# Kernel optimization log

Measured on AMD Instinct MI355X. Metric: run time of the kernel, lower is better.

The kernel has to match this reference:

```python
import jax, jax.numpy as jnp
import numpy as np

B, T = 16, 8192
L, RC, DC, SC, EC, E, NC = 16, 32, 32, 256, 256, 100, 256


def conv1d(x, w, b, dilation=1):
    # x: [B, Cin, T], w: [Cout, Cin, K], b: [Cout]
    y = jax.lax.conv_general_dilated(
        x, w, window_strides=(1,), padding='VALID',
        rhs_dilation=(dilation,), dimension_numbers=('NCH', 'OIH', 'NCH'))
    return y + b[None, :, None]


def setup_inputs() -> dict:
    key = jax.random.key(0)
    ks = jax.random.split(key, 32)
    n = lambda k, shp: (jax.random.normal(k, shp) * 0.1).astype(jnp.float32)
    return dict(
        tokens=jax.random.randint(ks[0], (B, T), 0, NC),
        emb=n(ks[1], (NC, E)),
        init_w=n(ks[2], (RC, E, 1)), init_b=n(ks[3], (RC,)),
        dil_w=n(ks[4], (L, DC, RC, 2)), dil_b=n(ks[5], (L, DC)),
        filt_w=n(ks[6], (L, DC, DC, 2)), filt_b=n(ks[7], (L, DC)),
        gate_w=n(ks[8], (L, DC, DC, 2)), gate_b=n(ks[9], (L, DC)),
        res_w=n(ks[10], (L, RC, DC, 1)), res_b=n(ks[11], (L, RC)),
        skip_w=n(ks[12], (L, SC, DC, 1)), skip_b=n(ks[13], (L, SC)),
        end1_w=n(ks[14], (EC, SC, 1)), end1_b=n(ks[15], (EC,)),
        end2_w=n(ks[16], (EC, EC, 1)), end2_b=n(ks[17], (EC,)),
        fc1_w=n(ks[18], (128, 256)), fc1_b=n(ks[19], (128,)),
        fc2_w=n(ks[20], (128, 128)), fc2_b=n(ks[21], (128,)),
        fc3_w=n(ks[22], (64, 128)), fc3_b=n(ks[23], (64,)),
        fc4_w=n(ks[24], (NC, 64)), fc4_b=n(ks[25], (NC,)),
    )


def reference(tokens, emb, init_w, init_b, dil_w, dil_b, filt_w, filt_b,
              gate_w, gate_b, res_w, res_b, skip_w, skip_b,
              end1_w, end1_b, end2_w, end2_b,
              fc1_w, fc1_b, fc2_w, fc2_b, fc3_w, fc3_b, fc4_w, fc4_b):
    x = emb[tokens]                     # [B, T, E]
    x = jnp.transpose(x, (0, 2, 1))     # [B, E, T]
    x = conv1d(x, init_w, init_b)       # [B, RC, T]
    skip = None
    for i in range(L):
        d = 2 ** (i % 4)                # dilation resets each block of 4 layers
        xp = jnp.pad(x, ((0, 0), (0, 0), (d + 1, 0)))        # left pad d+1
        residual = conv1d(xp, dil_w[i], dil_b[i], dilation=d)  # [B, DC, T+1]
        f = jnp.tanh(conv1d(residual, filt_w[i], filt_b[i]))   # [B, DC, T]
        g = jax.nn.sigmoid(conv1d(residual, gate_w[i], gate_b[i]))
        x = f * g
        skip = conv1d(x, skip_w[i], skip_b[i])   # overwritten each layer (source bug, kept faithful)
        x = conv1d(x, res_w[i], res_b[i]) + residual[:, :, :-1]
    h = jax.nn.relu(conv1d(jax.nn.relu(skip), end1_w, end1_b))
    h = conv1d(h, end2_w, end2_b)       # [B, EC, T]
    h = h[:, :, -1]                     # [B, 256] last timestep only
    h = jax.nn.relu(h @ fc1_w.T + fc1_b)
    h = jax.nn.relu(h @ fc2_w.T + fc2_b)
    h = jax.nn.relu(h @ fc3_w.T + fc3_b)
    out = h @ fc4_w.T + fc4_b           # [B, NC]
    return out
```

## Files before the change

kernel.cpp:

```cpp
#include <hip/hip_runtime.h>


#define BB 16
#define TT 8192
#define LL 16
#define W0 77
#define NT 256

typedef __attribute__((ext_vector_type(8)))  short short8;
typedef __attribute__((ext_vector_type(16))) float float16;

#define MFMA_B16(a, b, c) __builtin_amdgcn_mfma_f32_32x32x16_bf16(a, b, c, 0, 0, 0)

__device__ __forceinline__ short f2bs(float f) {
  union { float ff; unsigned u; } v; v.ff = f;
  unsigned u = v.u;
  return (short)((u + 0x7FFFu + ((u >> 16) & 1u)) >> 16);
}
__device__ __forceinline__ float b2f(short h) {
  union { unsigned u; float f; } v;
  v.u = ((unsigned)(unsigned short)h) << 16; return v.f;
}
__device__ __forceinline__ unsigned cvtpk(float lo, float hi) {
  unsigned r;
  asm("v_cvt_pk_bf16_f32 %0, %1, %2" : "=v"(r) : "v"(lo), "v"(hi));
  return r;
}
__device__ __forceinline__ short8 mk8(unsigned a, unsigned b, unsigned c, unsigned d) {
  union { unsigned u[4]; short8 s; } z;
  z.u[0] = a; z.u[1] = b; z.u[2] = c; z.u[3] = d; return z.s;
}
__device__ __forceinline__ float u2f(unsigned u) {
  union { unsigned x; float f; } z; z.x = u; return z.f;
}
__device__ __forceinline__ void asmb(const unsigned* own, const unsigned* cr,
                                     int kh, unsigned* o) {
  #pragma unroll
  for (int h = 0; h < 2; h++) {
    o[4*h+0] = kh ? cr[4*h+2] : own[4*h+0];
    o[4*h+1] = kh ? cr[4*h+3] : own[4*h+1];
    o[4*h+2] = kh ? own[4*h+2] : cr[4*h+0];
    o[4*h+3] = kh ? own[4*h+3] : cr[4*h+1];
  }
}

__device__ __forceinline__ void afrag2(const short* src, int row, int kh, short8* out) {
  out[0] = *(const short8*)&src[row * 32 + 8 * kh];
  out[1] = *(const short8*)&src[row * 32 + 16 + 8 * kh];
}

__device__ __forceinline__ void load_chunk(
    int li, int cid, float* pf,
    const float* dil_w, const float* filt_w, const float* gate_w, const float* res_w)
{
  int mat = cid >> 7;
  int h = (cid >> 6) & 1, ln = cid & 63;
  int n = ln & 31, k2 = ln >> 5;
  int base = (li * 32 + n) * 32 + 16 * h + 8 * k2;
  if (mat == 6) {
    const float* p = res_w + base;
    #pragma unroll
    for (int j = 0; j < 8; j++) pf[j] = p[j];
  } else {
    const float* w = (mat < 2) ? dil_w : (mat < 4) ? filt_w : gate_w;
    const float* p = w + base * 2 + (mat & 1);
    #pragma unroll
    for (int j = 0; j < 8; j++) pf[j] = p[2 * j];
  }
}

__global__ __launch_bounds__(NT, 1) void wavenet_kernel(
    const int* __restrict__ tokens,
    const float* __restrict__ emb,
    const float* __restrict__ init_w, const float* __restrict__ init_b,
    const float* __restrict__ dil_w,  const float* __restrict__ dil_b,
    const float* __restrict__ filt_w, const float* __restrict__ filt_b,
    const float* __restrict__ gate_w, const float* __restrict__ gate_b,
    const float* __restrict__ res_w,  const float* __restrict__ res_b,
    const float* __restrict__ skip_w, const float* __restrict__ skip_b,
    const float* __restrict__ end1_w, const float* __restrict__ end1_b,
    const float* __restrict__ end2_w, const float* __restrict__ end2_b,
    const float* __restrict__ fc1_w,  const float* __restrict__ fc1_b,
    const float* __restrict__ fc2_w,  const float* __restrict__ fc2_b,
    const float* __restrict__ fc3_w,  const float* __restrict__ fc3_b,
    const float* __restrict__ fc4_w,  const float* __restrict__ fc4_b,
    float* __restrict__ out)
{
  __shared__ __align__(16) short bfw[2][7168];
  __shared__ __align__(16) float bias2[2][128];
  __shared__ __align__(16) short xbuf[W0 * 32];
  __shared__ __align__(16) short pool[8624];
  __shared__ int tok[W0];
  __shared__ __align__(16) float vecA[256], vecB[256];

  short* rb = pool;
  short* xm = pool + 2432;

  const int tid  = threadIdx.x;
  const int lane = tid & 63;
  const int wv   = tid >> 6;
  const int m    = lane & 31;
  const int kh   = lane >> 5;
  const int b    = blockIdx.x;

  if (tid < W0) tok[tid] = tokens[b * TT + (TT - 1 - tid)];
  __syncthreads();

  for (int cid = tid; cid < 77 * 14; cid += NT) {
    int u = cid / 14, s = cid % 14;
    const float* er = emb + tok[u] * 100 + s * 8;
    short8 v;
    if (s < 12) {
      #pragma unroll
      for (int j = 0; j < 8; j++) v[j] = f2bs(er[j]);
    } else if (s == 12) {
      #pragma unroll
      for (int j = 0; j < 4; j++) v[j] = f2bs(er[j]);
      #pragma unroll
      for (int j = 4; j < 8; j++) v[j] = 0;
    } else {
      #pragma unroll
      for (int j = 0; j < 8; j++) v[j] = 0;
    }
    *(short8*)&pool[u * 112 + s * 8] = v;
  }
  for (int cid = tid; cid < 896; cid += NT) {
    float pf[8];
    load_chunk(0, cid, pf, dil_w, filt_w, gate_w, res_w);
    short8 v;
    #pragma unroll
    for (int j = 0; j < 8; j++) v[j] = f2bs(pf[j]);
    *(short8*)&bfw[0][cid * 8] = v;
  }
  if (tid < 128) {
    const float* bsrc = (tid < 32) ? dil_b : (tid < 64) ? filt_b : (tid < 96) ? gate_b : res_b;
    bias2[0][tid] = bsrc[tid & 31];
  }
  __syncthreads();

  if (wv < 3) {
    short8 bi[7];
    #pragma unroll
    for (int s = 0; s < 7; s++) {
      const float* p = init_w + m * 100 + s * 16 + kh * 8;
      short8 v;
      if (s < 6) {
        #pragma unroll
        for (int j = 0; j < 8; j++) v[j] = f2bs(p[j]);
      } else if (kh == 0) {
        #pragma unroll
        for (int j = 0; j < 4; j++) v[j] = f2bs(p[j]);
        #pragma unroll
        for (int j = 4; j < 8; j++) v[j] = 0;
      } else {
        #pragma unroll
        for (int j = 0; j < 8; j++) v[j] = 0;
      }
      bi[s] = v;
    }
    const float binit = init_b[m];
    const int R = wv * 32;
    int u = R + m; if (u > 76) u = 76;
    float16 acc;
    #pragma unroll
    for (int r = 0; r < 16; r++) acc[r] = binit;
    #pragma unroll
    for (int s = 0; s < 7; s++) {
      short8 a = *(const short8*)&pool[u * 112 + s * 16 + kh * 8];
      acc = MFMA_B16(a, bi[s], acc);
    }
    #pragma unroll
    for (int r = 0; r < 16; r++) {
      int row = (r & 3) + 8 * (r >> 2) + 4 * kh;
      int uu = R + row;
      if (uu < W0) xbuf[uu * 32 + m] = f2bs(acc[r]);
    }
  }
  __syncthreads();

  int Win = W0;
  for (int i = 0; i < 11; i++) {
    const int d = 1 << (i & 3);
    const int Wout = Win - d - 1;
    const int T = (Wout + 32) >> 5;
    const short* bw = bfw[i & 1];
    const float* bs = bias2[i & 1];

    float pfo[4][8];
    float pbias = 0.f;
    const int nch = (tid < 128) ? 4 : 3;
    const bool oldpf = (T >= 3) && (i + 1 < LL);
    if (oldpf) {
      #pragma unroll
      for (int q = 0; q < 4; q++) {
        if (q < nch)
          load_chunk(i + 1, tid + q * NT, pfo[q], dil_w, filt_w, gate_w, res_w);
      }
      if (tid < 128) {
        const float* bsrc = (tid < 32) ? dil_b : (tid < 64) ? filt_b : (tid < 96) ? gate_b : res_b;
        pbias = bsrc[(i + 1) * 32 + (tid & 31)];
      }
    }
    const bool newpf = (T <= 2) && (i + 1 < LL) && (wv >= T);
    const int nP = NT - T * 64;
    const int ptid = tid - T * 64;
    float pfn[7][8];
    if (newpf) {
      #pragma unroll
      for (int q = 0; q < 7; q++) {
        int c = ptid + q * nP;
        if (c < 896) load_chunk(i + 1, c, pfn[q], dil_w, filt_w, gate_w, res_w);
      }
    }

    short8 BW[5][2];
    if (wv < T) {
      const int R = wv * 32;
      short8 B0[2], B1[2];
      #pragma unroll
      for (int h = 0; h < 2; h++) {
        B0[h] = *(const short8*)&bw[((0 * 2 + h) * 64 + lane) * 8];
        B1[h] = *(const short8*)&bw[((1 * 2 + h) * 64 + lane) * 8];
      }
      #pragma unroll
      for (int mt = 0; mt < 5; mt++)
        #pragma unroll
        for (int h = 0; h < 2; h++)
          BW[mt][h] = *(const short8*)&bw[(((mt + 2) * 2 + h) * 64 + lane) * 8];
      int vra = R + m + d; if (vra > Win - 1) vra = Win - 1;
      int vrz = R + m;     if (vrz > Win - 1) vrz = Win - 1;
      short8 aA[2], aZ[2];
      afrag2(xbuf, vra, kh, aA);
      afrag2(xbuf, vrz, kh, aZ);
      float16 acc;
      const float bc = bs[m];
      #pragma unroll
      for (int r = 0; r < 16; r++) acc[r] = bc;
      acc = MFMA_B16(aA[0], B0[0], acc);
      acc = MFMA_B16(aA[1], B0[1], acc);
      acc = MFMA_B16(aZ[0], B1[0], acc);
      acc = MFMA_B16(aZ[1], B1[1], acc);
      #pragma unroll
      for (int r = 0; r < 16; r++) {
        int row = (r & 3) + 8 * (r >> 2) + 4 * kh;
        int vr = R + row;
        if (vr <= Wout) rb[vr * 32 + m] = f2bs(acc[r]);
      }
    }
    if (T >= 2) {
      __syncthreads();
    } else {
      asm volatile("s_waitcnt lgkmcnt(0)" ::: "memory");
    }

    if (wv < T) {
      const int R = wv * 32;
      int r1 = R + m + 1; if (r1 > Wout) r1 = Wout;
      int r0 = R + m;     if (r0 > Wout) r0 = Wout;
      short8 a1[2], a0[2];
      afrag2(rb, r1, kh, a1);
      afrag2(rb, r0, kh, a0);
      float16 accF, accG;
      const float bf = bs[32 + m], bg = bs[64 + m];
      #pragma unroll
      for (int r = 0; r < 16; r++) { accF[r] = bf; accG[r] = bg; }
      accF = MFMA_B16(a1[0], BW[0][0], accF);
      accF = MFMA_B16(a1[1], BW[0][1], accF);
      accF = MFMA_B16(a0[0], BW[1][0], accF);
      accF = MFMA_B16(a0[1], BW[1][1], accF);
      accG = MFMA_B16(a1[0], BW[2][0], accG);
      accG = MFMA_B16(a1[1], BW[2][1], accG);
      accG = MFMA_B16(a0[0], BW[3][0], accG);
      accG = MFMA_B16(a0[1], BW[3][1], accG);
      #pragma unroll
      for (int r = 0; r < 16; r++) {
        int row = (r & 3) + 8 * (r >> 2) + 4 * kh;
        int uf = R + row;
        if (uf < Wout) {
          float u = __expf(-2.f * accF[r]);
          float v = __expf(-accG[r]);
          float fg = (1.f - u) * __builtin_amdgcn_rcpf((1.f + u) * (1.f + v));
          xm[uf * 32 + m] = f2bs(fg);
        }
      }
      asm volatile("s_waitcnt lgkmcnt(0)" ::: "memory");

      int rx = R + m; if (rx > Wout - 1) rx = Wout - 1;
      short8 aX[2];
      afrag2(xm, rx, kh, aX);
      float16 accX;
      const float br = bs[96 + m];
      #pragma unroll
      for (int r = 0; r < 16; r++) {
        int row = (r & 3) + 8 * (r >> 2) + 4 * kh;
        int rr = R + row + 1; if (rr > Wout) rr = Wout;
        accX[r] = br + b2f(rb[rr * 32 + m]);
      }
      accX = MFMA_B16(aX[0], BW[4][0], accX);
      accX = MFMA_B16(aX[1], BW[4][1], accX);
      #pragma unroll
      for (int r = 0; r < 16; r++) {
        int row = (r & 3) + 8 * (r >> 2) + 4 * kh;
        int uf = R + row;
        if (uf < Wout) xbuf[uf * 32 + m] = f2bs(accX[r]);
      }
    } else if (newpf) {
      short* dst = bfw[(i + 1) & 1];
      #pragma unroll
      for (int q = 0; q < 7; q++) {
        int c = ptid + q * nP;
        if (c < 896) {
          short8 v;
          #pragma unroll
          for (int j = 0; j < 8; j++) v[j] = f2bs(pfn[q][j]);
          *(short8*)&dst[c * 8] = v;
        }
      }
      for (int t2 = ptid; t2 < 128; t2 += nP) {
        const float* bsrc = (t2 < 32) ? dil_b : (t2 < 64) ? filt_b : (t2 < 96) ? gate_b : res_b;
        bias2[(i + 1) & 1][t2] = bsrc[(i + 1) * 32 + (t2 & 31)];
      }
    }

    if (oldpf) {
      short* dst = bfw[(i + 1) & 1];
      #pragma unroll
      for (int q = 0; q < 4; q++) {
        if (q < nch) {
          short8 v;
          #pragma unroll
          for (int j = 0; j < 8; j++) v[j] = f2bs(pfo[q][j]);
          *(short8*)&dst[(tid + q * NT) * 8] = v;
        }
      }
      if (tid < 128) bias2[(i + 1) & 1][tid] = pbias;
    }
    __syncthreads();
    Win = Wout;
  }

  {
    const int t31 = lane & 31;
    const int hb  = lane & 32;
    unsigned xcur[8];
    if (wv == 0) {
      int tcl = t31 < Win - 1 ? t31 : Win - 1;
      #pragma unroll
      for (int h = 0; h < 2; h++) {
        short8 v = *(const short8*)&xbuf[tcl * 32 + 16 * h + 8 * kh];
        union { short8 s; unsigned u[4]; } z; z.s = v;
        #pragma unroll
        for (int s = 0; s < 4; s++) xcur[4 * h + s] = z.u[s];
      }
    }

    #pragma unroll
    for (int i = 11; i < LL; i++) {
      const int d = 1 << (i & 3);
      const int Wout = Win - d - 1;
      const short* bw = bfw[i & 1];
      const float* bs = bias2[i & 1];

      const bool npf = (i + 1 < LL) && (wv >= 1);
      const int ptid = tid - 64;
      float pfn[7][8];
      if (npf) {
        #pragma unroll
        for (int q = 0; q < 7; q++) {
          int c = ptid + q * 192;
          if (c < 896) load_chunk(i + 1, c, pfn[q], dil_w, filt_w, gate_w, res_w);
        }
      }

      if (wv == 0) {
        short8 WA[7][2];
        #pragma unroll
        for (int mt = 0; mt < 7; mt++)
          #pragma unroll
          for (int h = 0; h < 2; h++)
            WA[mt][h] = *(const short8*)&bw[((mt * 2 + h) * 64 + lane) * 8];

        int td = t31 + d; if (td > Win - 1) td = Win - 1;
        int srcd = hb | td;
        unsigned xd[8];
        #pragma unroll
        for (int q = 0; q < 8; q++) xd[q] = (unsigned)__shfl((int)xcur[q], srcd);
        float16 acc;
        #pragma unroll
        for (int g = 0; g < 4; g++) {
          float4 b4 = *(const float4*)&bs[4 * kh + 8 * g];
          acc[4*g+0] = b4.x; acc[4*g+1] = b4.y; acc[4*g+2] = b4.z; acc[4*g+3] = b4.w;
        }
        acc = MFMA_B16(WA[0][0], mk8(xd[0], xd[1], xd[2], xd[3]), acc);
        acc = MFMA_B16(WA[0][1], mk8(xd[4], xd[5], xd[6], xd[7]), acc);
        acc = MFMA_B16(WA[1][0], mk8(xcur[0], xcur[1], xcur[2], xcur[3]), acc);
        acc = MFMA_B16(WA[1][1], mk8(xcur[4], xcur[5], xcur[6], xcur[7]), acc);

        unsigned wrb[8], xc[8], x1[8], x1c[8];
        #pragma unroll
        for (int q = 0; q < 8; q++) wrb[q] = cvtpk(acc[2 * q], acc[2 * q + 1]);
        int t1 = t31 + 1; if (t1 > Wout) t1 = Wout;
        int s1o = hb | t1;
        int s1c = (hb ^ 32) | t1;
        #pragma unroll
        for (int q = 0; q < 8; q++) {
          xc[q]  = (unsigned)__shfl((int)wrb[q], lane ^ 32);
          x1[q]  = (unsigned)__shfl((int)wrb[q], s1o);
          x1c[q] = (unsigned)__shfl((int)wrb[q], s1c);
        }
        unsigned rb0w[8], rb1w[8];
        asmb(wrb, xc, kh, rb0w);
        asmb(x1, x1c, kh, rb1w);

        float16 accF, accG;
        #pragma unroll
        for (int g = 0; g < 4; g++) {
          float4 bF = *(const float4*)&bs[32 + 4 * kh + 8 * g];
          float4 bG = *(const float4*)&bs[64 + 4 * kh + 8 * g];
          accF[4*g+0] = bF.x; accF[4*g+1] = bF.y; accF[4*g+2] = bF.z; accF[4*g+3] = bF.w;
          accG[4*g+0] = bG.x; accG[4*g+1] = bG.y; accG[4*g+2] = bG.z; accG[4*g+3] = bG.w;
        }
        short8 RB10 = mk8(rb1w[0], rb1w[1], rb1w[2], rb1w[3]);
        short8 RB11 = mk8(rb1w[4], rb1w[5], rb1w[6], rb1w[7]);
        short8 RB00 = mk8(rb0w[0], rb0w[1], rb0w[2], rb0w[3]);
        short8 RB01 = mk8(rb0w[4], rb0w[5], rb0w[6], rb0w[7]);
        accF = MFMA_B16(WA[2][0], RB10, accF);
        accF = MFMA_B16(WA[2][1], RB11, accF);
        accF = MFMA_B16(WA[3][0], RB00, accF);
        accF = MFMA_B16(WA[3][1], RB01, accF);
        accG = MFMA_B16(WA[4][0], RB10, accG);
        accG = MFMA_B16(WA[4][1], RB11, accG);
        accG = MFMA_B16(WA[5][0], RB00, accG);
        accG = MFMA_B16(WA[5][1], RB01, accG);
        float fg[16];
        #pragma unroll
        for (int r = 0; r < 16; r++) {
          float u = __expf(-2.f * accF[r]);
          float v = __expf(-accG[r]);
          fg[r] = (1.f - u) * __builtin_amdgcn_rcpf((1.f + u) * (1.f + v));
        }
        unsigned wxm[8];
        #pragma unroll
        for (int q = 0; q < 8; q++) wxm[q] = cvtpk(fg[2 * q], fg[2 * q + 1]);

        if (i == LL - 1) {
          if (t31 == 0) {
            #pragma unroll
            for (int q = 0; q < 8; q++) {
              int c0 = (2 * q & 3) + 8 * (q >> 1) + 4 * kh;
              *(unsigned*)&xm[c0] = wxm[q];
            }
          }
        } else {
          unsigned xmc[8];
          #pragma unroll
          for (int q = 0; q < 8; q++) xmc[q] = (unsigned)__shfl((int)wxm[q], lane ^ 32);
          unsigned xmw[8];
          asmb(wxm, xmc, kh, xmw);
          float16 accX;
          #pragma unroll
          for (int g = 0; g < 4; g++) {
            float4 bR = *(const float4*)&bs[96 + 4 * kh + 8 * g];
            #pragma unroll
            for (int j = 0; j < 4; j++) {
              int r = 4 * g + j;
              unsigned w = x1[r >> 1];
              float rv = (r & 1) ? u2f(w & 0xFFFF0000u) : u2f(w << 16);
              accX[r] = ((const float*)&bR)[j] + rv;
            }
          }
          accX = MFMA_B16(WA[6][0], mk8(xmw[0], xmw[1], xmw[2], xmw[3]), accX);
          accX = MFMA_B16(WA[6][1], mk8(xmw[4], xmw[5], xmw[6], xmw[7]), accX);
          unsigned wxn[8], xnc[8];
          #pragma unroll
          for (int q = 0; q < 8; q++) wxn[q] = cvtpk(accX[2 * q], accX[2 * q + 1]);
          #pragma unroll
          for (int q = 0; q < 8; q++) xnc[q] = (unsigned)__shfl((int)wxn[q], lane ^ 32);
          asmb(wxn, xnc, kh, xcur);
        }
      } else if (npf) {
        short* dst = bfw[(i + 1) & 1];
        #pragma unroll
        for (int q = 0; q < 7; q++) {
          int c = ptid + q * 192;
          if (c < 896) {
            short8 v;
            #pragma unroll
            for (int j = 0; j < 8; j++) v[j] = f2bs(pfn[q][j]);
            *(short8*)&dst[c * 8] = v;
          }
        }
        for (int t2 = ptid; t2 < 128; t2 += 192) {
          const float* bsrc = (t2 < 32) ? dil_b : (t2 < 64) ? filt_b : (t2 < 96) ? gate_b : res_b;
          bias2[(i + 1) & 1][t2] = bsrc[(i + 1) * 32 + (t2 & 31)];
        }
      }
      __syncthreads();
      Win = Wout;
    }
  }

  {
    float acc = skip_b[15 * 256 + tid];
    const float* wr = skip_w + (15 * 256 + tid) * 32;
    #pragma unroll
    for (int k = 0; k < 32; k += 4) {
      float4 w = *(const float4*)&wr[k];
      acc += (w.x * b2f(xm[k]) + w.y * b2f(xm[k+1])) + (w.z * b2f(xm[k+2]) + w.w * b2f(xm[k+3]));
    }
    vecA[tid] = fmaxf(acc, 0.f);
  }
  __syncthreads();
  {
    const float* wr = end1_w + tid * 256;
    float a4[4] = {0.f, 0.f, 0.f, 0.f};
    #pragma unroll 4
    for (int k = 0; k < 256; k += 16) {
      #pragma unroll
      for (int q = 0; q < 4; q++) {
        float4 w = *(const float4*)&wr[k + 4 * q];
        float4 a = *(const float4*)&vecA[k + 4 * q];
        a4[q] += (w.x * a.x + w.y * a.y) + (w.z * a.z + w.w * a.w);
      }
    }
    vecB[tid] = fmaxf(end1_b[tid] + (a4[0] + a4[1]) + (a4[2] + a4[3]), 0.f);
  }
  __syncthreads();
  float h2;
  {
    const float* wr = end2_w + tid * 256;
    float a4[4] = {0.f, 0.f, 0.f, 0.f};
    #pragma unroll 4
    for (int k = 0; k < 256; k += 16) {
      #pragma unroll
      for (int q = 0; q < 4; q++) {
        float4 w = *(const float4*)&wr[k + 4 * q];
        float4 a = *(const float4*)&vecB[k + 4 * q];
        a4[q] += (w.x * a.x + w.y * a.y) + (w.z * a.z + w.w * a.w);
      }
    }
    h2 = end2_b[tid] + (a4[0] + a4[1]) + (a4[2] + a4[3]);
  }
  __syncthreads();
  vecA[tid] = h2;
  __syncthreads();
  if (tid < 128) {
    const float* wr = fc1_w + tid * 256;
    float a4[4] = {0.f, 0.f, 0.f, 0.f};
    #pragma unroll 4
    for (int k = 0; k < 256; k += 16) {
      #pragma unroll
      for (int q = 0; q < 4; q++) {
        float4 w = *(const float4*)&wr[k + 4 * q];
        float4 a = *(const float4*)&vecA[k + 4 * q];
        a4[q] += (w.x * a.x + w.y * a.y) + (w.z * a.z + w.w * a.w);
      }
    }
    vecB[tid] = fmaxf(fc1_b[tid] + (a4[0] + a4[1]) + (a4[2] + a4[3]), 0.f);
  }
  __syncthreads();
  if (tid < 128) {
    const float* wr = fc2_w + tid * 128;
    float a4[4] = {0.f, 0.f, 0.f, 0.f};
    #pragma unroll 2
    for (int k = 0; k < 128; k += 16) {
      #pragma unroll
      for (int q = 0; q < 4; q++) {
        float4 w = *(const float4*)&wr[k + 4 * q];
        float4 a = *(const float4*)&vecB[k + 4 * q];
        a4[q] += (w.x * a.x + w.y * a.y) + (w.z * a.z + w.w * a.w);
      }
    }
    vecA[tid] = fmaxf(fc2_b[tid] + (a4[0] + a4[1]) + (a4[2] + a4[3]), 0.f);
  }
  __syncthreads();
  if (tid < 64) {
    const float* wr = fc3_w + tid * 128;
    float a4[4] = {0.f, 0.f, 0.f, 0.f};
    #pragma unroll 2
    for (int k = 0; k < 128; k += 16) {
      #pragma unroll
      for (int q = 0; q < 4; q++) {
        float4 w = *(const float4*)&wr[k + 4 * q];
        float4 a = *(const float4*)&vecA[k + 4 * q];
        a4[q] += (w.x * a.x + w.y * a.y) + (w.z * a.z + w.w * a.w);
      }
    }
    vecB[tid] = fmaxf(fc3_b[tid] + (a4[0] + a4[1]) + (a4[2] + a4[3]), 0.f);
  }
  __syncthreads();
  {
    const float* wr = fc4_w + tid * 64;
    float a4[4] = {0.f, 0.f, 0.f, 0.f};
    #pragma unroll
    for (int k = 0; k < 64; k += 16) {
      #pragma unroll
      for (int q = 0; q < 4; q++) {
        float4 w = *(const float4*)&wr[k + 4 * q];
        float4 a = *(const float4*)&vecB[k + 4 * q];
        a4[q] += (w.x * a.x + w.y * a.y) + (w.z * a.z + w.w * a.w);
      }
    }
    out[b * 256 + tid] = fc4_b[tid] + (a4[0] + a4[1]) + (a4[2] + a4[3]);
  }
}

extern "C" void kernel_launch(void* const* d_in, const int* in_sizes, int n_in,
                              void* d_out, int out_size, void* d_ws, size_t ws_size,
                              hipStream_t stream) {
  wavenet_kernel<<<BB, NT, 0, stream>>>(
      (const int*)d_in[0],    (const float*)d_in[1],  (const float*)d_in[2],  (const float*)d_in[3],
      (const float*)d_in[4],  (const float*)d_in[5],  (const float*)d_in[6],  (const float*)d_in[7],
      (const float*)d_in[8],  (const float*)d_in[9],  (const float*)d_in[10], (const float*)d_in[11],
      (const float*)d_in[12], (const float*)d_in[13], (const float*)d_in[14], (const float*)d_in[15],
      (const float*)d_in[16], (const float*)d_in[17], (const float*)d_in[18], (const float*)d_in[19],
      (const float*)d_in[20], (const float*)d_in[21], (const float*)d_in[22], (const float*)d_in[23],
      (const float*)d_in[24], (const float*)d_in[25], (float*)d_out);
}
```

Baseline: 205.0 us.

## Overlap 31-row wave tiles to drop intra-layer barrier, double-buffer xbuf

Each wave now owns a 31-row output tile that overlaps its neighbour by one row, so the dilated conv result a wave writes is the only data it later reads. This replaces the block-wide __syncthreads between the dilated and filter/gate stages with a local lgkmcnt wait. The residual output goes into a second, double-buffered xbuf so layers no longer read and write the same buffer. The single-wave shuffle path now starts one layer earlier (layer 10), pulling rows 32 and 33 from shared memory for the out-of-range lanes. The price is one redundant row of work per wave, possibly an extra wave in the early layers, and more shared memory. The tail dense-layer loops are also unrolled further and one barrier is removed.

Result: no change. 204.9 us (-0.0%).

```diff
diff --git a/kernel.cpp b/kernel.cpp
--- a/kernel.cpp
+++ b/kernel.cpp
@@ -47,6 +47,16 @@
 __device__ __forceinline__ void afrag2(const short* src, int row, int kh, short8* out) {
   out[0] = *(const short8*)&src[row * 32 + 8 * kh];
   out[1] = *(const short8*)&src[row * 32 + 16 + 8 * kh];
+}
+
+__device__ __forceinline__ void ldrow(const short* xb, int row, int kh, unsigned* w8) {
+  #pragma unroll
+  for (int h = 0; h < 2; h++) {
+    short8 v = *(const short8*)&xb[row * 32 + 16 * h + 8 * kh];
+    union { short8 s; unsigned u[4]; } z; z.s = v;
+    #pragma unroll
+    for (int s = 0; s < 4; s++) w8[4 * h + s] = z.u[s];
+  }
 }
 
 __device__ __forceinline__ void load_chunk(
@@ -88,7 +98,7 @@
 {
   __shared__ __align__(16) short bfw[2][7168];
   __shared__ __align__(16) float bias2[2][128];
-  __shared__ __align__(16) short xbuf[W0 * 32];
+  __shared__ __align__(16) short xbuf[2][W0 * 32];
   __shared__ __align__(16) short pool[8624];
   __shared__ int tok[W0];
   __shared__ __align__(16) float vecA[256], vecB[256];
@@ -173,18 +183,20 @@
     for (int r = 0; r < 16; r++) {
       int row = (r & 3) + 8 * (r >> 2) + 4 * kh;
       int uu = R + row;
-      if (uu < W0) xbuf[uu * 32 + m] = f2bs(acc[r]);
+      if (uu < W0) xbuf[0][uu * 32 + m] = f2bs(acc[r]);
     }
   }
   __syncthreads();
 
   int Win = W0;
-  for (int i = 0; i < 11; i++) {
+  for (int i = 0; i < 10; i++) {
     const int d = 1 << (i & 3);
     const int Wout = Win - d - 1;
-    const int T = (Wout + 32) >> 5;
+    const int T = (Wout + 31) / 31;
     const short* bw = bfw[i & 1];
     const float* bs = bias2[i & 1];
+    const short* xin  = xbuf[i & 1];
+    short* xout = xbuf[(i + 1) & 1];
 
     float pfo[4][8];
     float pbias = 0.f;
@@ -213,10 +225,9 @@
       }
     }
 
-    short8 BW[5][2];
     if (wv < T) {
-      const int R = wv * 32;
-      short8 B0[2], B1[2];
+      const int R = wv * 31;
+      short8 B0[2], B1[2], BW[5][2];
       #pragma unroll
       for (int h = 0; h < 2; h++) {
         B0[h] = *(const short8*)&bw[((0 * 2 + h) * 64 + lane) * 8];
@@ -227,11 +238,12 @@
         #pragma unroll
         for (int h = 0; h < 2; h++)
           BW[mt][h] = *(const short8*)&bw[(((mt + 2) * 2 + h) * 64 + lane) * 8];
+
       int vra = R + m + d; if (vra > Win - 1) vra = Win - 1;
       int vrz = R + m;     if (vrz > Win - 1) vrz = Win - 1;
       short8 aA[2], aZ[2];
-      afrag2(xbuf, vra, kh, aA);
-      afrag2(xbuf, vrz, kh, aZ);
+      afrag2(xin, vra, kh, aA);
+      afrag2(xin, vrz, kh, aZ);
       float16 acc;
       const float bc = bs[m];
       #pragma unroll
@@ -246,16 +258,10 @@
         int vr = R + row;
         if (vr <= Wout) rb[vr * 32 + m] = f2bs(acc[r]);
       }
-    }
-    if (T >= 2) {
-      __syncthreads();
-    } else {
       asm volatile("s_waitcnt lgkmcnt(0)" ::: "memory");
-    }
-
-    if (wv < T) {
-      const int R = wv * 32;
-      int r1 = R + m + 1; if (r1 > Wout) r1 = Wout;
+
+      const int capA = (R + 31 < Wout) ? (R + 31) : Wout;
+      int r1 = R + m + 1; if (r1 > capA) r1 = capA;
       int r0 = R + m;     if (r0 > Wout) r0 = Wout;
       short8 a1[2], a0[2];
       afrag2(rb, r1, kh, a1);
@@ -276,7 +282,7 @@
       for (int r = 0; r < 16; r++) {
         int row = (r & 3) + 8 * (r >> 2) + 4 * kh;
         int uf = R + row;
-        if (uf < Wout) {
+        if (row < 31 && uf < Wout) {
           float u = __expf(-2.f * accF[r]);
           float v = __expf(-accG[r]);
           float fg = (1.f - u) * __builtin_amdgcn_rcpf((1.f + u) * (1.f + v));
@@ -285,7 +291,8 @@
       }
       asm volatile("s_waitcnt lgkmcnt(0)" ::: "memory");
 
-      int rx = R + m; if (rx > Wout - 1) rx = Wout - 1;
+      const int capX = (R + 30 < Wout - 1) ? (R + 30) : (Wout - 1);
+      int rx = R + m; if (rx > capX) rx = capX;
       short8 aX[2];
       afrag2(xm, rx, kh, aX);
       float16 accX;
@@ -302,7 +309,7 @@
       for (int r = 0; r < 16; r++) {
         int row = (r & 3) + 8 * (r >> 2) + 4 * kh;
         int uf = R + row;
-        if (uf < Wout) xbuf[uf * 32 + m] = f2bs(accX[r]);
+        if (row < 31 && uf < Wout) xout[uf * 32 + m] = f2bs(accX[r]);
       }
     } else if (newpf) {
       short* dst = bfw[(i + 1) & 1];
@@ -342,20 +349,17 @@
   {
     const int t31 = lane & 31;
     const int hb  = lane & 32;
-    unsigned xcur[8];
+    unsigned xcur[8], e32[8], e33[8];
     if (wv == 0) {
+      const short* xb0 = xbuf[0];
       int tcl = t31 < Win - 1 ? t31 : Win - 1;
-      #pragma unroll
-      for (int h = 0; h < 2; h++) {
-        short8 v = *(const short8*)&xbuf[tcl * 32 + 16 * h + 8 * kh];
-        union { short8 s; unsigned u[4]; } z; z.s = v;
-        #pragma unroll
-        for (int s = 0; s < 4; s++) xcur[4 * h + s] = z.u[s];
-      }
-    }
-
-    #pragma unroll
-    for (int i = 11; i < LL; i++) {
+      ldrow(xb0, tcl, kh, xcur);
+      ldrow(xb0, 32, kh, e32);
+      ldrow(xb0, 33, kh, e33);
+    }
+
+    #pragma unroll
+    for (int i = 10; i < LL; i++) {
       const int d = 1 << (i & 3);
       const int Wout = Win - d - 1;
       const short* bw = bfw[i & 1];
@@ -380,11 +384,23 @@
           for (int h = 0; h < 2; h++)
             WA[mt][h] = *(const short8*)&bw[((mt * 2 + h) * 64 + lane) * 8];
 
-        int td = t31 + d; if (td > Win - 1) td = Win - 1;
-        int srcd = hb | td;
         unsigned xd[8];
-        #pragma unroll
-        for (int q = 0; q < 8; q++) xd[q] = (unsigned)__shfl((int)xcur[q], srcd);
+        if (i == 10) {
+          int td = t31 + d;
+          int ts = td > 31 ? 31 : td;
+          #pragma unroll
+          for (int q = 0; q < 8; q++) {
+            unsigned s = (unsigned)__shfl((int)xcur[q], hb | ts);
+            s = (td == 32) ? e32[q] : s;
+            s = (td >= 33) ? e33[q] : s;
+            xd[q] = s;
+          }
+        } else {
+          int td = t31 + d; if (td > Win - 1) td = Win - 1;
+          int srcd = hb | td;
+          #pragma unroll
+          for (int q = 0; q < 8; q++) xd[q] = (unsigned)__shfl((int)xcur[q], srcd);
+        }
         float16 acc;
         #pragma unroll
         for (int g = 0; g < 4; g++) {
@@ -514,7 +530,7 @@
   {
     const float* wr = end1_w + tid * 256;
     float a4[4] = {0.f, 0.f, 0.f, 0.f};
-    #pragma unroll 4
+    #pragma unroll 8
     for (int k = 0; k < 256; k += 16) {
       #pragma unroll
       for (int q = 0; q < 4; q++) {
@@ -526,11 +542,10 @@
     vecB[tid] = fmaxf(end1_b[tid] + (a4[0] + a4[1]) + (a4[2] + a4[3]), 0.f);
   }
   __syncthreads();
-  float h2;
   {
     const float* wr = end2_w + tid * 256;
     float a4[4] = {0.f, 0.f, 0.f, 0.f};
-    #pragma unroll 4
+    #pragma unroll 8
     for (int k = 0; k < 256; k += 16) {
       #pragma unroll
       for (int q = 0; q < 4; q++) {
@@ -539,15 +554,14 @@
         a4[q] += (w.x * a.x + w.y * a.y) + (w.z * a.z + w.w * a.w);
       }
     }
-    h2 = end2_b[tid] + (a4[0] + a4[1]) + (a4[2] + a4[3]);
-  }
-  __syncthreads();
-  vecA[tid] = h2;
+    float h2 = end2_b[tid] + (a4[0] + a4[1]) + (a4[2] + a4[3]);
+    vecA[tid] = h2;
+  }
   __syncthreads();
   if (tid < 128) {
     const float* wr = fc1_w + tid * 256;
     float a4[4] = {0.f, 0.f, 0.f, 0.f};
-    #pragma unroll 4
+    #pragma unroll 8
     for (int k = 0; k < 256; k += 16) {
       #pragma unroll
       for (int q = 0; q < 4; q++) {
@@ -562,7 +576,7 @@
   if (tid < 128) {
     const float* wr = fc2_w + tid * 128;
     float a4[4] = {0.f, 0.f, 0.f, 0.f};
-    #pragma unroll 2
+    #pragma unroll 4
     for (int k = 0; k < 128; k += 16) {
       #pragma unroll
       for (int q = 0; q < 4; q++) {
@@ -577,7 +591,7 @@
   if (tid < 64) {
     const float* wr = fc3_w + tid * 128;
     float a4[4] = {0.f, 0.f, 0.f, 0.f};
-    #pragma unroll 2
+    #pragma unroll 4
     for (int k = 0; k < 128; k += 16) {
       #pragma unroll
       for (int q = 0; q < 4; q++) {
```
